# Kernel tuning notes

Measured on AMD Instinct MI355X. Metric: run time of the kernel, lower is better.

The kernel has to match this reference:

```python
import jax, jax.numpy as jnp
import numpy as np
import math

B, S, D, H = 4, 2048, 1024, 16
HD = D // H

def setup_inputs() -> dict:
    key = jax.random.key(0)
    ks = jax.random.split(key, 12)
    sc = 1.0 / math.sqrt(D)
    inp = {
        'q': jax.random.normal(ks[0], (B, S, D), jnp.float32),
        'k': jax.random.normal(ks[1], (B, S, D), jnp.float32),
        'v': jax.random.normal(ks[2], (B, S, D), jnp.float32),
        # causal mask: 1.0 where attention is disallowed (j > i)
        'mask': jnp.broadcast_to(jnp.triu(jnp.ones((S, S), jnp.float32), k=1), (B, S, S)),
        'Wq': jax.random.normal(ks[3], (D, D), jnp.float32) * sc,
        'bq': jnp.zeros((D,), jnp.float32),
        'Wk': jax.random.normal(ks[4], (D, D), jnp.float32) * sc,
        'bk': jnp.zeros((D,), jnp.float32),
        'Wv': jax.random.normal(ks[5], (D, D), jnp.float32) * sc,
        'bv': jnp.zeros((D,), jnp.float32),
        'Wo': jax.random.normal(ks[6], (D, D), jnp.float32) * sc,
        'bo': jnp.zeros((D,), jnp.float32),
    }
    return inp

def reference(q, k, v, mask, Wq, bq, Wk, bk, Wv, bv, Wo, bo):
    # linear projections (torch Linear: x @ W^T + b)
    qp = q @ Wq.T + bq
    kp = k @ Wk.T + bk
    vp = v @ Wv.T + bv
    # split heads: [B,S,D] -> [B,H,S,hd]
    qh = qp.reshape(B, S, H, HD).transpose(0, 2, 1, 3)
    kh = kp.reshape(B, S, H, HD).transpose(0, 2, 1, 3)
    vh = vp.reshape(B, S, H, HD).transpose(0, 2, 1, 3)
    scores = jnp.einsum('bhqd,bhkd->bhqk', qh, kh) / jnp.sqrt(jnp.float32(HD))
    scores = scores + mask[:, None, :, :] * jnp.float32(-100000.0)
    attn = jax.nn.softmax(scores, axis=-1)
    out = jnp.einsum('bhqk,bhkd->bhqd', attn, vh)
    out = out.transpose(0, 2, 1, 3).reshape(B, S, D)
    out = out @ Wo.T + bo
    return (out, kh, vh)
```

## Files before the change

### kernel.cpp

```cpp
#include <hip/hip_runtime.h>
#include <stdint.h>

#define Bn 4
#define Sn 2048
#define Dn 1024
#define Hn 16
#define HDn 64

typedef unsigned short u16;
typedef unsigned int u32;
typedef __attribute__((ext_vector_type(8))) __bf16 bf16x8;
typedef __attribute__((ext_vector_type(4))) float f32x4;
typedef __attribute__((ext_vector_type(16))) float f32x16;
typedef __attribute__((ext_vector_type(4))) u32 u32x4;

#define CEXP 0.18033688011112042f

#define EXP2F(x) __builtin_amdgcn_exp2f(x)

__device__ __forceinline__ u16 f2bf(float f) {
  union { float f; u32 u; } x; x.f = f;
  u32 r = x.u + 0x7FFFu + ((x.u >> 16) & 1u);
  return (u16)(r >> 16);
}

__device__ __forceinline__ void gload16(const u16* g, u16* l) {
  __builtin_amdgcn_global_load_lds(
      (const __attribute__((address_space(1))) void*)g,
      (__attribute__((address_space(3))) void*)l, 16, 0, 0);
}

__global__ void cvt3_kernel(const float* __restrict__ a, const float* __restrict__ b,
                            const float* __restrict__ c,
                            u16* __restrict__ oa, u16* __restrict__ ob,
                            u16* __restrict__ oc) {
  const float* in = (blockIdx.y == 0) ? a : (blockIdx.y == 1) ? b : c;
  u16* out = (blockIdx.y == 0) ? oa : (blockIdx.y == 1) ? ob : oc;
  int i = blockIdx.x * 256 + threadIdx.x;
  float4 v = ((const float4*)in)[i];
  ushort4 o;
  o.x = f2bf(v.x); o.y = f2bf(v.y); o.z = f2bf(v.z); o.w = f2bf(v.w);
  ((ushort4*)out)[i] = o;
}

__global__ void cvt4_kernel(const float* __restrict__ a, const float* __restrict__ b,
                            const float* __restrict__ c, const float* __restrict__ d,
                            u16* __restrict__ oa, u16* __restrict__ ob,
                            u16* __restrict__ oc, u16* __restrict__ od) {
  const float* in = (blockIdx.y == 0) ? a : (blockIdx.y == 1) ? b
                   : (blockIdx.y == 2) ? c : d;
  u16* out = (blockIdx.y == 0) ? oa : (blockIdx.y == 1) ? ob
            : (blockIdx.y == 2) ? oc : od;
  int i = blockIdx.x * 256 + threadIdx.x;
  float4 v = ((const float4*)in)[i];
  ushort4 o;
  o.x = f2bf(v.x); o.y = f2bf(v.y); o.z = f2bf(v.z); o.w = f2bf(v.w);
  ((ushort4*)out)[i] = o;
}

template<int MODE>
__global__ __launch_bounds__(256, 2) void gemm_bt(
    const u16* __restrict__ A, const u16* __restrict__ W,
    const float* __restrict__ bias,
    float* __restrict__ outF, u16* __restrict__ outB)
{
  __shared__ u16 As[2][4096];
  __shared__ u16 Bs[2][4096];

  const int t = threadIdx.x, w = t >> 6, lane = t & 63;
  int bid = (int)blockIdx.x;
  bid = (bid & 7) * 64 + (bid >> 3);
  const int m0 = (bid >> 3) * 128, n0 = (bid & 7) * 128;
  const int wm = (w >> 1) * 64, wn = (w & 1) * 64;
  const int lrow = lane & 15;

  f32x4 acc[4][4] = {};

  auto stage = [&](int buf, int k0) {
    #pragma unroll
    for (int i = 0; i < 2; ++i) {
      const int c = i * 256 + t;
      const int row = c >> 2;
      const int off = ((c & 3) ^ (row & 3)) * 8;
      gload16(A + (size_t)(m0 + row) * 1024 + k0 + off, &As[buf][(c & ~63) * 8]);
      gload16(W + (size_t)(n0 + row) * 1024 + k0 + off, &Bs[buf][(c & ~63) * 8]);
    }
  };

  stage(0, 0);
  for (int kt = 0; kt < 32; ++kt) {
    const int buf = kt & 1;
    __syncthreads();
    if (kt < 31) stage(buf ^ 1, (kt + 1) * 32);
    bf16x8 a[4], b[4];
    #pragma unroll
    for (int i = 0; i < 4; ++i) {
      const int ra = wm + i * 16 + lrow;
      const int rb = wn + i * 16 + lrow;
      a[i] = *(const bf16x8*)&As[buf][ra * 32 + (((lane >> 4) ^ (ra & 3)) * 8)];
      b[i] = *(const bf16x8*)&Bs[buf][rb * 32 + (((lane >> 4) ^ (rb & 3)) * 8)];
    }
    #pragma unroll
    for (int i = 0; i < 4; ++i)
      #pragma unroll
      for (int j = 0; j < 4; ++j)
        acc[i][j] = __builtin_amdgcn_mfma_f32_16x16x32_bf16(a[i], b[j], acc[i][j], 0, 0, 0);
  }

  const int g4 = (lane >> 4) * 4;
  #pragma unroll
  for (int i = 0; i < 4; ++i) {
    #pragma unroll
    for (int j = 0; j < 4; ++j) {
      const int gn = n0 + wn + j * 16 + lrow;
      const float bv = bias[gn];
      #pragma unroll
      for (int r = 0; r < 4; ++r) {
        const int gm = m0 + wm + i * 16 + g4 + r;
        const float x = acc[i][j][r] + bv;
        if (MODE == 3) {
          outF[(size_t)gm * 1024 + gn] = x;
        } else {
          const int b_ = gm >> 11, s_ = gm & 2047, h_ = gn >> 6, d_ = gn & 63;
          const size_t hidx = (((size_t)b_ * Hn + h_) * Sn + s_) * HDn + d_;
          if (MODE == 0) outB[hidx] = f2bf(x * CEXP);
          if (MODE == 1) { outF[hidx] = x; outB[hidx] = f2bf(x); }
          if (MODE == 2) { outF[hidx] = x;
                           outB[(((size_t)b_ * Hn + h_) * HDn + d_) * Sn + s_] = f2bf(x); }
        }
      }
    }
  }
}

__global__ __launch_bounds__(256, 4) void attn_kernel(
    const u16* __restrict__ qh, const u16* __restrict__ kh,
    const u16* __restrict__ vt, u16* __restrict__ ao)
{
  __shared__ u16 Ks[2][4096];
  __shared__ u16 Vs[2][4096];

  const int t = threadIdx.x, w = t >> 6, lane = t & 63;
  const int bid = (int)blockIdx.x;
  const int k_ = bid >> 8;
  const int x_ = bid & 7;
  const int c_ = (bid >> 3) & 31;
  const int bh = x_ * 8 + (c_ >> 2);
  const int cq = c_ & 3;
  const int p = (k_ == 0) ? (15 - cq) : (k_ == 1) ? (8 + cq)
              : (k_ == 2) ? (7 - cq) : cq;
  const int l31 = lane & 31, h = lane >> 5;

  const u16* Kb = kh + (size_t)bh * Sn * HDn;
  const u16* Vb = vt + (size_t)bh * HDn * Sn;
  const u16* Qb = qh + (size_t)bh * Sn * HDn;

  const int q0w = p * 128 + w * 32;
  const int qg = q0w + l31;
  const int NT = 2 * p + 2;
  const int NTw = ((q0w + 31) >> 6) + 1;

  bf16x8 qf[4];
  #pragma unroll
  for (int kk = 0; kk < 4; ++kk)
    qf[kk] = *(const bf16x8*)(Qb + (size_t)qg * HDn + kk * 16 + h * 8);

  float m = -1e30f, l = 0.f;
  f32x16 o0 = {}, o1 = {};

  const int c0 = t, c1 = t + 256;
  const int kr0 = ((c0 >> 8) << 5) + (c0 & 31), kr1 = ((c1 >> 8) << 5) + (c1 & 31);
  const u16* kSrc0 = Kb + (size_t)kr0 * HDn + ((c0 >> 6) & 3) * 16 + ((c0 >> 5) & 1) * 8;
  const u16* kSrc1 = Kb + (size_t)kr1 * HDn + ((c1 >> 6) & 3) * 16 + ((c1 >> 5) & 1) * 8;
  const u16* vSrc0 = Vb + (size_t)kr0 * Sn + (2 * ((c0 >> 6) & 3) + ((c0 >> 5) & 1)) * 8;
  const u16* vSrc1 = Vb + (size_t)kr1 * Sn + (2 * ((c1 >> 6) & 3) + ((c1 >> 5) & 1)) * 8;
  const int d0 = (c0 & ~63) * 8, d1 = (c1 & ~63) * 8;

  auto stage = [&](int buf) {
    gload16(kSrc0, &Ks[buf][d0]);
    gload16(kSrc1, &Ks[buf][d1]);
    gload16(vSrc0, &Vs[buf][d0]);
    gload16(vSrc1, &Vs[buf][d1]);
    kSrc0 += 64 * HDn; kSrc1 += 64 * HDn;
    vSrc0 += 64;       vSrc1 += 64;
  };

  auto unit = [&](int buf, int jt) {
    const u16* Kbuf = &Ks[buf][0];
    const u16* Vbuf = &Vs[buf][0];
    f32x16 s0 = {}, s1 = {};

    __builtin_amdgcn_s_setprio(1);
    #pragma unroll
    for (int kk = 0; kk < 4; ++kk) {
      bf16x8 k0 = *(const bf16x8*)&Kbuf[(kk * 64 + lane) * 8];
      bf16x8 k1 = *(const bf16x8*)&Kbuf[((4 + kk) * 64 + lane) * 8];
      s0 = __builtin_amdgcn_mfma_f32_32x32x16_bf16(k0, qf[kk], s0, 0, 0, 0);
      s1 = __builtin_amdgcn_mfma_f32_32x32x16_bf16(k1, qf[kk], s1, 0, 0, 0);
    }
    __builtin_amdgcn_s_setprio(0);

    if (jt * 64 + 63 > q0w) {
      const int kvb = jt * 64 + 4 * h;
      #pragma unroll
      for (int r = 0; r < 16; ++r) {
        const int rho = (r & 3) + 8 * (r >> 2);
        s0[r] = (kvb + rho > qg) ? -1e30f : s0[r];
        s1[r] = (kvb + 32 + rho > qg) ? -1e30f : s1[r];
      }
    }

    float mx = s0[0];
    #pragma unroll
    for (int r = 1; r < 16; ++r) mx = fmaxf(mx, s0[r]);
    #pragma unroll
    for (int r = 0; r < 16; ++r) mx = fmaxf(mx, s1[r]);
    mx = fmaxf(mx, __shfl_xor(mx, 32, 64));

    if (__any(mx > m + 11.5415603f)) {
      const float mn = fmaxf(m, mx);
      const float al = EXP2F(m - mn);
      m = mn; l *= al;
      #pragma unroll
      for (int r = 0; r < 16; ++r) { o0[r] *= al; o1[r] *= al; }
    }

    float sum = 0.f;
    #pragma unroll
    for (int r = 0; r < 16; ++r) { s0[r] = EXP2F(s0[r] - m); sum += s0[r]; }
    #pragma unroll
    for (int r = 0; r < 16; ++r) { s1[r] = EXP2F(s1[r] - m); sum += s1[r]; }
    sum += __shfl_xor(sum, 32, 64);
    l += sum;

    u32 w0[8], w1[8];
    #pragma unroll
    for (int i = 0; i < 8; ++i) {
      asm("v_cvt_pk_bf16_f32 %0, %1, %2" : "=v"(w0[i]) : "v"(s0[2 * i]), "v"(s0[2 * i + 1]));
      asm("v_cvt_pk_bf16_f32 %0, %1, %2" : "=v"(w1[i]) : "v"(s1[2 * i]), "v"(s1[2 * i + 1]));
    }
    asm("v_permlane32_swap_b32 %0, %1" : "+v"(w0[0]), "+v"(w0[2]));
    asm("v_permlane32_swap_b32 %0, %1" : "+v"(w0[1]), "+v"(w0[3]));
    asm("v_permlane32_swap_b32 %0, %1" : "+v"(w0[4]), "+v"(w0[6]));
    asm("v_permlane32_swap_b32 %0, %1" : "+v"(w0[5]), "+v"(w0[7]));
    asm("v_permlane32_swap_b32 %0, %1" : "+v"(w1[0]), "+v"(w1[2]));
    asm("v_permlane32_swap_b32 %0, %1" : "+v"(w1[1]), "+v"(w1[3]));
    asm("v_permlane32_swap_b32 %0, %1" : "+v"(w1[4]), "+v"(w1[6]));
    asm("v_permlane32_swap_b32 %0, %1" : "+v"(w1[5]), "+v"(w1[7]));

    __builtin_amdgcn_s_setprio(1);
    #pragma unroll
    for (int s = 0; s < 4; ++s) {
      const u32* wt = (s < 2) ? w0 : w1;
      const int j4 = (s & 1) * 4;
      u32x4 fr = { wt[j4], wt[j4 + 1], wt[j4 + 2], wt[j4 + 3] };
      bf16x8 pf = __builtin_bit_cast(bf16x8, fr);
      bf16x8 v0 = *(const bf16x8*)&Vbuf[(s * 64 + lane) * 8];
      bf16x8 v1 = *(const bf16x8*)&Vbuf[((4 + s) * 64 + lane) * 8];
      o0 = __builtin_amdgcn_mfma_f32_32x32x16_bf16(v0, pf, o0, 0, 0, 0);
      o1 = __builtin_amdgcn_mfma_f32_32x32x16_bf16(v1, pf, o1, 0, 0, 0);
    }
    __builtin_amdgcn_s_setprio(0);
  };

  stage(0);
  for (int jt = 0; jt < NT; ++jt) {
    const int buf = jt & 1;
    __syncthreads();
    if (jt + 1 < NT) stage(buf ^ 1);
    if (jt < NTw) unit(buf, jt);
  }

  const int b_ = bh >> 4, h_ = bh & 15;
  const float rl = 1.0f / l;
  u16* base = ao + ((size_t)b_ * Sn + qg) * Dn + h_ * HDn;
  #pragma unroll
  for (int n = 0; n < 2; ++n)
    #pragma unroll
    for (int u = 0; u < 4; ++u) {
      const f32x16& o = n ? o1 : o0;
      ushort4 ov;
      ov.x = f2bf(o[4 * u + 0] * rl); ov.y = f2bf(o[4 * u + 1] * rl);
      ov.z = f2bf(o[4 * u + 2] * rl); ov.w = f2bf(o[4 * u + 3] * rl);
      *(ushort4*)&base[n * 32 + 8 * u + 4 * h] = ov;
    }
}

extern "C" void kernel_launch(void* const* d_in, const int* in_sizes, int n_in,
                              void* d_out, int out_size, void* d_ws, size_t ws_size,
                              hipStream_t stream)
{
  const float* q  = (const float*)d_in[0];
  const float* k  = (const float*)d_in[1];
  const float* v  = (const float*)d_in[2];
  const float* Wq = (const float*)d_in[4];
  const float* bq = (const float*)d_in[5];
  const float* Wk = (const float*)d_in[6];
  const float* bk = (const float*)d_in[7];
  const float* Wv = (const float*)d_in[8];
  const float* bv = (const float*)d_in[9];
  const float* Wo = (const float*)d_in[10];
  const float* bo = (const float*)d_in[11];

  float* out_o  = (float*)d_out;
  float* out_kh = out_o + (size_t)Bn * Sn * Dn;
  float* out_vh = out_kh + (size_t)Bn * Sn * Dn;

  char* ws = (char*)d_ws;
  const size_t MB = 1ull << 20;
  u16* wq_bf = (u16*)(ws + 0 * MB);
  u16* wk_bf = (u16*)(ws + 2 * MB);
  u16* wv_bf = (u16*)(ws + 4 * MB);
  u16* wo_bf = (u16*)(ws + 6 * MB);
  u16* q_bf  = (u16*)(ws + 8 * MB);
  u16* k_bf  = (u16*)(ws + 24 * MB);
  u16* v_bf  = (u16*)(ws + 40 * MB);
  u16* qh_bf = (u16*)(ws + 56 * MB);
  u16* kh_bf = (u16*)(ws + 72 * MB);
  u16* vt_bf = (u16*)(ws + 88 * MB);
  u16* ao_bf = q_bf;

  const int NC = Bn * Sn * Dn / 4;
  cvt3_kernel<<<dim3(NC / 256, 3), 256, 0, stream>>>(q, k, v, q_bf, k_bf, v_bf);
  const int NW = Dn * Dn / 4;
  cvt4_kernel<<<dim3(NW / 256, 4), 256, 0, stream>>>(Wq, Wk, Wv, Wo,
                                                     wq_bf, wk_bf, wv_bf, wo_bf);

  gemm_bt<0><<<512, 256, 0, stream>>>(q_bf, wq_bf, bq, nullptr, qh_bf);
  gemm_bt<1><<<512, 256, 0, stream>>>(k_bf, wk_bf, bk, out_kh, kh_bf);
  gemm_bt<2><<<512, 256, 0, stream>>>(v_bf, wv_bf, bv, out_vh, vt_bf);

  attn_kernel<<<1024, 256, 0, stream>>>(qh_bf, kh_bf, vt_bf, ao_bf);

  gemm_bt<3><<<512, 256, 0, stream>>>(ao_bf, wo_bf, bo, out_o, nullptr);
}
```

Baseline: 209.1 us.

## Merge QKV GEMMs into one launch and shrink attention blocks to single-buffered 64-row tiles

The three Q/K/V projection GEMMs become one kernel launch of 1536 blocks that picks its operands by block index. Launch bounds on the GEMMs rise to allow more resident blocks. The attention kernel now uses 128-thread blocks covering 64 query rows each, launched as 2048 blocks paired for causal load balance, with a single-buffered K/V LDS tile. This aims to cut launch overhead and improve occupancy and tail balance, but it loses the double-buffered prefetch overlap in attention, adding two barriers per tile.

Measured after the change: 255.3 us. +22.1%, slower.

```diff
diff --git a/kernel.cpp b/kernel.cpp
--- a/kernel.cpp
+++ b/kernel.cpp
@@ -58,11 +58,87 @@
   ((ushort4*)out)[i] = o;
 }
 
-template<int MODE>
-__global__ __launch_bounds__(256, 2) void gemm_bt(
+__global__ __launch_bounds__(256, 4) void gemm_qkv(
+    const u16* __restrict__ Aq, const u16* __restrict__ Ak, const u16* __restrict__ Av,
+    const u16* __restrict__ Wqp, const u16* __restrict__ Wkp, const u16* __restrict__ Wvp,
+    const float* __restrict__ bqp, const float* __restrict__ bkp, const float* __restrict__ bvp,
+    float* __restrict__ kF, float* __restrict__ vF,
+    u16* __restrict__ qB, u16* __restrict__ kB, u16* __restrict__ vB)
+{
+  __shared__ u16 As[2][4096];
+  __shared__ u16 Bs[2][4096];
+
+  const int t = threadIdx.x, w = t >> 6, lane = t & 63;
+  int bid = (int)blockIdx.x;
+  bid = (bid & 7) * 192 + (bid >> 3);
+  const int nb = bid >> 6, mb = bid & 63;
+  const int sel = nb >> 3;
+  const int m0 = mb * 128, n0 = (nb & 7) * 128;
+  const int wm = (w >> 1) * 64, wn = (w & 1) * 64;
+  const int lrow = lane & 15;
+
+  const u16* A = (sel == 0) ? Aq : (sel == 1) ? Ak : Av;
+  const u16* W = (sel == 0) ? Wqp : (sel == 1) ? Wkp : Wvp;
+  const float* bias = (sel == 0) ? bqp : (sel == 1) ? bkp : bvp;
+
+  f32x4 acc[4][4] = {};
+
+  auto stage = [&](int buf, int k0) {
+    #pragma unroll
+    for (int i = 0; i < 2; ++i) {
+      const int c = i * 256 + t;
+      const int row = c >> 2;
+      const int off = ((c & 3) ^ (row & 3)) * 8;
+      gload16(A + (size_t)(m0 + row) * 1024 + k0 + off, &As[buf][(c & ~63) * 8]);
+      gload16(W + (size_t)(n0 + row) * 1024 + k0 + off, &Bs[buf][(c & ~63) * 8]);
+    }
+  };
+
+  stage(0, 0);
+  for (int kt = 0; kt < 32; ++kt) {
+    const int buf = kt & 1;
+    __syncthreads();
+    if (kt < 31) stage(buf ^ 1, (kt + 1) * 32);
+    bf16x8 a[4], b[4];
+    #pragma unroll
+    for (int i = 0; i < 4; ++i) {
+      const int ra = wm + i * 16 + lrow;
+      const int rb = wn + i * 16 + lrow;
+      a[i] = *(const bf16x8*)&As[buf][ra * 32 + (((lane >> 4) ^ (ra & 3)) * 8)];
+      b[i] = *(const bf16x8*)&Bs[buf][rb * 32 + (((lane >> 4) ^ (rb & 3)) * 8)];
+    }
+    #pragma unroll
+    for (int i = 0; i < 4; ++i)
+      #pragma unroll
+      for (int j = 0; j < 4; ++j)
+        acc[i][j] = __builtin_amdgcn_mfma_f32_16x16x32_bf16(a[i], b[j], acc[i][j], 0, 0, 0);
+  }
+
+  const int g4 = (lane >> 4) * 4;
+  #pragma unroll
+  for (int i = 0; i < 4; ++i) {
+    #pragma unroll
+    for (int j = 0; j < 4; ++j) {
+      const int gn = n0 + wn + j * 16 + lrow;
+      const float bv = bias[gn];
+      #pragma unroll
+      for (int r = 0; r < 4; ++r) {
+        const int gm = m0 + wm + i * 16 + g4 + r;
+        const float x = acc[i][j][r] + bv;
+        const int b_ = gm >> 11, s_ = gm & 2047, h_ = gn >> 6, d_ = gn & 63;
+        const size_t hidx = (((size_t)b_ * Hn + h_) * Sn + s_) * HDn + d_;
+        if (sel == 0) qB[hidx] = f2bf(x * CEXP);
+        if (sel == 1) { kF[hidx] = x; kB[hidx] = f2bf(x); }
+        if (sel == 2) { vF[hidx] = x;
+                        vB[(((size_t)b_ * Hn + h_) * HDn + d_) * Sn + s_] = f2bf(x); }
+      }
+    }
+  }
+}
+
+__global__ __launch_bounds__(256, 4) void gemm_out(
     const u16* __restrict__ A, const u16* __restrict__ W,
-    const float* __restrict__ bias,
-    float* __restrict__ outF, u16* __restrict__ outB)
+    const float* __restrict__ bias, float* __restrict__ outF)
 {
   __shared__ u16 As[2][4096];
   __shared__ u16 Bs[2][4096];
@@ -109,7 +185,7 @@
 
   const int g4 = (lane >> 4) * 4;
   #pragma unroll
-  for (int i = 0; i < 4; ++i) {
+  for (int i = 0; i < 4; ++i)
     #pragma unroll
     for (int j = 0; j < 4; ++j) {
       const int gn = n0 + wn + j * 16 + lrow;
@@ -117,48 +193,35 @@
       #pragma unroll
       for (int r = 0; r < 4; ++r) {
         const int gm = m0 + wm + i * 16 + g4 + r;
-        const float x = acc[i][j][r] + bv;
-        if (MODE == 3) {
-          outF[(size_t)gm * 1024 + gn] = x;
-        } else {
-          const int b_ = gm >> 11, s_ = gm & 2047, h_ = gn >> 6, d_ = gn & 63;
-          const size_t hidx = (((size_t)b_ * Hn + h_) * Sn + s_) * HDn + d_;
-          if (MODE == 0) outB[hidx] = f2bf(x * CEXP);
-          if (MODE == 1) { outF[hidx] = x; outB[hidx] = f2bf(x); }
-          if (MODE == 2) { outF[hidx] = x;
-                           outB[(((size_t)b_ * Hn + h_) * HDn + d_) * Sn + s_] = f2bf(x); }
-        }
+        outF[(size_t)gm * 1024 + gn] = acc[i][j][r] + bv;
       }
     }
-  }
-}
-
-__global__ __launch_bounds__(256, 4) void attn_kernel(
+}
+
+__global__ __launch_bounds__(128, 4) void attn_kernel(
     const u16* __restrict__ qh, const u16* __restrict__ kh,
     const u16* __restrict__ vt, u16* __restrict__ ao)
 {
-  __shared__ u16 Ks[2][4096];
-  __shared__ u16 Vs[2][4096];
+  __shared__ u16 Ks[4096];
+  __shared__ u16 Vs[4096];
 
   const int t = threadIdx.x, w = t >> 6, lane = t & 63;
   const int bid = (int)blockIdx.x;
-  const int k_ = bid >> 8;
   const int x_ = bid & 7;
   const int c_ = (bid >> 3) & 31;
+  const int r_ = bid >> 8;
   const int bh = x_ * 8 + (c_ >> 2);
-  const int cq = c_ & 3;
-  const int p = (k_ == 0) ? (15 - cq) : (k_ == 1) ? (8 + cq)
-              : (k_ == 2) ? (7 - cq) : cq;
+  const int s_ = 4 * (c_ & 3) + (r_ >> 1);
+  const int tq = (r_ & 1) ? (31 - s_) : s_;
   const int l31 = lane & 31, h = lane >> 5;
 
   const u16* Kb = kh + (size_t)bh * Sn * HDn;
   const u16* Vb = vt + (size_t)bh * HDn * Sn;
   const u16* Qb = qh + (size_t)bh * Sn * HDn;
 
-  const int q0w = p * 128 + w * 32;
+  const int q0w = tq * 64 + w * 32;
   const int qg = q0w + l31;
-  const int NT = 2 * p + 2;
-  const int NTw = ((q0w + 31) >> 6) + 1;
+  const int NT = tq + 1;
 
   bf16x8 qf[4];
   #pragma unroll
@@ -168,33 +231,42 @@
   float m = -1e30f, l = 0.f;
   f32x16 o0 = {}, o1 = {};
 
-  const int c0 = t, c1 = t + 256;
-  const int kr0 = ((c0 >> 8) << 5) + (c0 & 31), kr1 = ((c1 >> 8) << 5) + (c1 & 31);
-  const u16* kSrc0 = Kb + (size_t)kr0 * HDn + ((c0 >> 6) & 3) * 16 + ((c0 >> 5) & 1) * 8;
-  const u16* kSrc1 = Kb + (size_t)kr1 * HDn + ((c1 >> 6) & 3) * 16 + ((c1 >> 5) & 1) * 8;
-  const u16* vSrc0 = Vb + (size_t)kr0 * Sn + (2 * ((c0 >> 6) & 3) + ((c0 >> 5) & 1)) * 8;
-  const u16* vSrc1 = Vb + (size_t)kr1 * Sn + (2 * ((c1 >> 6) & 3) + ((c1 >> 5) & 1)) * 8;
-  const int d0 = (c0 & ~63) * 8, d1 = (c1 & ~63) * 8;
-
-  auto stage = [&](int buf) {
-    gload16(kSrc0, &Ks[buf][d0]);
-    gload16(kSrc1, &Ks[buf][d1]);
-    gload16(vSrc0, &Vs[buf][d0]);
-    gload16(vSrc1, &Vs[buf][d1]);
-    kSrc0 += 64 * HDn; kSrc1 += 64 * HDn;
-    vSrc0 += 64;       vSrc1 += 64;
+  const u16* kS0; const u16* kS1; const u16* kS2; const u16* kS3;
+  const u16* vS0; const u16* vS1; const u16* vS2; const u16* vS3;
+  int dst0, dst1, dst2, dst3;
+  {
+    #define SRCS(i, KS, VS, DS)                                            \
+      { const int c = t + (i) * 128;                                       \
+        const int kr = ((c >> 8) << 5) + (c & 31);                         \
+        const int col = ((c >> 6) & 3) * 16 + ((c >> 5) & 1) * 8;          \
+        KS = Kb + (size_t)kr * HDn + col;                                  \
+        VS = Vb + (size_t)kr * Sn + col;                                   \
+        DS = (c & ~63) * 8; }
+    SRCS(0, kS0, vS0, dst0) SRCS(1, kS1, vS1, dst1)
+    SRCS(2, kS2, vS2, dst2) SRCS(3, kS3, vS3, dst3)
+    #undef SRCS
+  }
+
+  auto stage = [&]() {
+    gload16(kS0, &Ks[dst0]); gload16(kS1, &Ks[dst1]);
+    gload16(kS2, &Ks[dst2]); gload16(kS3, &Ks[dst3]);
+    gload16(vS0, &Vs[dst0]); gload16(vS1, &Vs[dst1]);
+    gload16(vS2, &Vs[dst2]); gload16(vS3, &Vs[dst3]);
+    kS0 += 64 * HDn; kS1 += 64 * HDn; kS2 += 64 * HDn; kS3 += 64 * HDn;
+    vS0 += 64; vS1 += 64; vS2 += 64; vS3 += 64;
   };
 
-  auto unit = [&](int buf, int jt) {
-    const u16* Kbuf = &Ks[buf][0];
-    const u16* Vbuf = &Vs[buf][0];
+  for (int jt = 0; jt < NT; ++jt) {
+    __syncthreads();
+    stage();
+    __syncthreads();
+
     f32x16 s0 = {}, s1 = {};
-
     __builtin_amdgcn_s_setprio(1);
     #pragma unroll
     for (int kk = 0; kk < 4; ++kk) {
-      bf16x8 k0 = *(const bf16x8*)&Kbuf[(kk * 64 + lane) * 8];
-      bf16x8 k1 = *(const bf16x8*)&Kbuf[((4 + kk) * 64 + lane) * 8];
+      bf16x8 k0 = *(const bf16x8*)&Ks[(kk * 64 + lane) * 8];
+      bf16x8 k1 = *(const bf16x8*)&Ks[((4 + kk) * 64 + lane) * 8];
       s0 = __builtin_amdgcn_mfma_f32_32x32x16_bf16(k0, qf[kk], s0, 0, 0, 0);
       s1 = __builtin_amdgcn_mfma_f32_32x32x16_bf16(k1, qf[kk], s1, 0, 0, 0);
     }
@@ -255,20 +327,12 @@
       const int j4 = (s & 1) * 4;
       u32x4 fr = { wt[j4], wt[j4 + 1], wt[j4 + 2], wt[j4 + 3] };
       bf16x8 pf = __builtin_bit_cast(bf16x8, fr);
-      bf16x8 v0 = *(const bf16x8*)&Vbuf[(s * 64 + lane) * 8];
-      bf16x8 v1 = *(const bf16x8*)&Vbuf[((4 + s) * 64 + lane) * 8];
+      bf16x8 v0 = *(const bf16x8*)&Vs[(s * 64 + lane) * 8];
+      bf16x8 v1 = *(const bf16x8*)&Vs[((4 + s) * 64 + lane) * 8];
       o0 = __builtin_amdgcn_mfma_f32_32x32x16_bf16(v0, pf, o0, 0, 0, 0);
       o1 = __builtin_amdgcn_mfma_f32_32x32x16_bf16(v1, pf, o1, 0, 0, 0);
     }
     __builtin_amdgcn_s_setprio(0);
-  };
-
-  stage(0);
-  for (int jt = 0; jt < NT; ++jt) {
-    const int buf = jt & 1;
-    __syncthreads();
-    if (jt + 1 < NT) stage(buf ^ 1);
-    if (jt < NTw) unit(buf, jt);
   }
 
   const int b_ = bh >> 4, h_ = bh & 15;
@@ -326,11 +390,13 @@
   cvt4_kernel<<<dim3(NW / 256, 4), 256, 0, stream>>>(Wq, Wk, Wv, Wo,
                                                      wq_bf, wk_bf, wv_bf, wo_bf);
 
-  gemm_bt<0><<<512, 256, 0, stream>>>(q_bf, wq_bf, bq, nullptr, qh_bf);
-  gemm_bt<1><<<512, 256, 0, stream>>>(k_bf, wk_bf, bk, out_kh, kh_bf);
-  gemm_bt<2><<<512, 256, 0, stream>>>(v_bf, wv_bf, bv, out_vh, vt_bf);
-
-  attn_kernel<<<1024, 256, 0, stream>>>(qh_bf, kh_bf, vt_bf, ao_bf);
-
-  gemm_bt<3><<<512, 256, 0, stream>>>(ao_bf, wo_bf, bo, out_o, nullptr);
-}
+  gemm_qkv<<<1536, 256, 0, stream>>>(q_bf, k_bf, v_bf,
+                                     wq_bf, wk_bf, wv_bf,
+                                     bq, bk, bv,
+                                     out_kh, out_vh,
+                                     qh_bf, kh_bf, vt_bf);
+
+  attn_kernel<<<2048, 128, 0, stream>>>(qh_bf, kh_bf, vt_bf, ao_bf);
+
+  gemm_out<<<512, 256, 0, stream>>>(ao_bf, wo_bf, bo, out_o);
+}
```
